# Kernel optimization log

Measured on AMD Instinct MI355X. Metric: run time of the kernel, lower is better.

## Reference

```python
import jax, jax.numpy as jnp
import numpy as np

NUM_HEADS = 8
NUM_GROUPS = 32
EPS = 1e-5


def setup_inputs() -> dict:
    key = jax.random.key(0)
    ks = jax.random.split(key, 7)
    B, C, H, W = 8, 512, 32, 32
    x = jax.random.normal(ks[0], (B, C, H, W), dtype=jnp.float32)
    # GroupNorm affine params
    gn_w = jnp.ones((C,), dtype=jnp.float32)
    gn_b = jnp.zeros((C,), dtype=jnp.float32)
    # 1x1 conv == linear over channel dim; store squeezed weights (out, in)
    qkv_w = jax.random.normal(ks[1], (3 * C, C), dtype=jnp.float32) * (1.0 / np.sqrt(C))
    qkv_b = jnp.zeros((3 * C,), dtype=jnp.float32)
    proj_w = jax.random.normal(ks[2], (C, C), dtype=jnp.float32) * (1.0 / np.sqrt(C))
    proj_b = jnp.zeros((C,), dtype=jnp.float32)
    return {"x": x, "gn_w": gn_w, "gn_b": gn_b, "qkv_w": qkv_w,
            "qkv_b": qkv_b, "proj_w": proj_w, "proj_b": proj_b}


def reference(x, gn_w, gn_b, qkv_w, qkv_b, proj_w, proj_b):
    B, C, H, W = x.shape
    G = NUM_GROUPS
    hd = C // NUM_HEADS
    scale = hd ** -0.5
    # GroupNorm: normalize over (C//G, H, W) per group
    xg = x.reshape(B, G, C // G, H, W)
    mean = xg.mean(axis=(2, 3, 4), keepdims=True)
    var = xg.var(axis=(2, 3, 4), keepdims=True)
    xn = ((xg - mean) * jax.lax.rsqrt(var + EPS)).reshape(B, C, H, W)
    xn = xn * gn_w[None, :, None, None] + gn_b[None, :, None, None]
    # QKV 1x1 conv
    qkv = jnp.einsum('bchw,oc->bohw', xn, qkv_w) + qkv_b[None, :, None, None]
    # (B, 3, heads, head_dim, HW) -> (3, B, heads, HW, head_dim)
    qkv = qkv.reshape(B, 3, NUM_HEADS, hd, H * W).transpose(1, 0, 2, 4, 3)
    q, k, v = qkv[0], qkv[1], qkv[2]
    attn = jax.nn.softmax(jnp.einsum('bhqd,bhkd->bhqk', q, k) * scale, axis=-1)
    out = jnp.einsum('bhqk,bhkd->bhqd', attn, v)  # (B, heads, HW, hd)
    out = out.transpose(0, 1, 3, 2).reshape(B, C, H, W)
    out = jnp.einsum('bchw,oc->bohw', out, proj_w) + proj_b[None, :, None, None]
    return out + x
```

## Files before the change

kernel.cpp:

```cpp
#include <hip/hip_runtime.h>
#include <hip/hip_bf16.h>
#include <math.h>

typedef __bf16 bf16_t;
typedef __bf16 bf16x8 __attribute__((ext_vector_type(8)));
typedef __bf16 bf16x4 __attribute__((ext_vector_type(4)));
typedef float  f32x4  __attribute__((ext_vector_type(4)));
typedef short  short4v __attribute__((ext_vector_type(4)));

#define NB    8
#define NC    512
#define NHW   1024
#define NHEAD 8
#define NHD   64
#define NG    32
#define NCG   16
#define NO3   1536

__device__ __forceinline__ void lds_load16(bf16_t* lds, const bf16_t* g) {
  __builtin_amdgcn_global_load_lds(
      (__attribute__((address_space(1))) unsigned int*)(g),
      (__attribute__((address_space(3))) unsigned int*)(void*)(lds),
      16, 0, 0);
}

__device__ __forceinline__ f32x4 mfma16(bf16x4 a, bf16x4 b, f32x4 c) {
#if __has_builtin(__builtin_amdgcn_mfma_f32_16x16x16bf16_1k)
  return __builtin_amdgcn_mfma_f32_16x16x16bf16_1k(
      __builtin_bit_cast(short4v, a), __builtin_bit_cast(short4v, b), c, 0, 0, 0);
#else
  f32x4 d;
  asm("v_mfma_f32_16x16x16_bf16 %0, %1, %2, %3"
      : "=v"(d) : "v"(a), "v"(b), "v"(c));
  return d;
#endif
}

__global__ __launch_bounds__(256)
void gn_kernel(const float* __restrict__ x, const float* __restrict__ gw,
               const float* __restrict__ gb, bf16_t* __restrict__ xn)
{
  const int bg = blockIdx.x;
  const int b = bg >> 5, g = bg & 31;
  const float* xp = x + ((size_t)b * NC + g * NCG) * NHW;
  const int tid = threadIdx.x;
  const int wave = tid >> 6, lane = tid & 63;

  float s1 = 0.f, s2 = 0.f;
  const float4* xp4 = (const float4*)xp;
  for (int i = tid; i < 4096; i += 256) {
    float4 v = xp4[i];
    s1 += v.x + v.y + v.z + v.w;
    s2 += v.x * v.x + v.y * v.y + v.z * v.z + v.w * v.w;
  }
  for (int off = 32; off > 0; off >>= 1) {
    s1 += __shfl_down(s1, off);
    s2 += __shfl_down(s2, off);
  }
  __shared__ float red[16];
  if (lane == 0) { red[wave] = s1; red[8 + wave] = s2; }
  __syncthreads();
  float tot1 = red[0] + red[1] + red[2] + red[3];
  float tot2 = red[8] + red[9] + red[10] + red[11];
  const float mean = tot1 * (1.0f / 16384.0f);
  const float var  = tot2 * (1.0f / 16384.0f) - mean * mean;
  const float rstd = rsqrtf(var + 1e-5f);

  float gam[NCG], bet[NCG];
  #pragma unroll
  for (int c = 0; c < NCG; ++c) {
    gam[c] = gw[g * NCG + c] * rstd;
    bet[c] = gb[g * NCG + c] - mean * gam[c];
  }
  bf16_t* op = xn + (size_t)b * NHW * NC + g * NCG;
  for (int s = tid; s < NHW; s += 256) {
    __align__(16) bf16_t vals[NCG];
    #pragma unroll
    for (int c = 0; c < NCG; ++c)
      vals[c] = (bf16_t)(xp[c * NHW + s] * gam[c] + bet[c]);
    *(bf16x8*)(op + (size_t)s * NC)     = *(const bf16x8*)&vals[0];
    *(bf16x8*)(op + (size_t)s * NC + 8) = *(const bf16x8*)&vals[8];
  }
}

__global__ __launch_bounds__(256)
void wconv_kernel(const float* __restrict__ qw, const float* __restrict__ pw,
                  bf16_t* __restrict__ qwb, bf16_t* __restrict__ pwb)
{
  const int gid = blockIdx.x * 256 + threadIdx.x;
  const int n1 = NO3 * NC / 4;
  float4 v; bf16x4 o;
  if (gid < n1) {
    v = ((const float4*)qw)[gid];
    o[0] = (bf16_t)v.x; o[1] = (bf16_t)v.y; o[2] = (bf16_t)v.z; o[3] = (bf16_t)v.w;
    ((bf16x4*)qwb)[gid] = o;
  } else {
    int g2 = gid - n1;
    v = ((const float4*)pw)[g2];
    o[0] = (bf16_t)v.x; o[1] = (bf16_t)v.y; o[2] = (bf16_t)v.z; o[3] = (bf16_t)v.w;
    ((bf16x4*)pwb)[g2] = o;
  }
}

__device__ __forceinline__ void gemm_mainloop(const bf16_t* Ap, const bf16_t* Bp,
                                              bf16_t* sA, bf16_t* sB, f32x4 (&acc)[4][4])
{
  const int tid = threadIdx.x;
  const int wave = tid >> 6, lane = tid & 63;
  const int quad = lane >> 4, l16 = lane & 15;
  const int wm = wave >> 1, wn = wave & 1;
  for (int k0 = 0; k0 < 512; k0 += 32) {
    #pragma unroll
    for (int j = 0; j < 2; ++j) {
      int c = wave * 64 + j * 256 + lane;
      int row = c >> 2, ko = (c & 3) * 8;
      lds_load16(sA + (size_t)(wave * 64 + j * 256) * 8, Ap + (size_t)row * 512 + k0 + ko);
      lds_load16(sB + (size_t)(wave * 64 + j * 256) * 8, Bp + (size_t)row * 512 + k0 + ko);
    }
    __syncthreads();
    bf16x8 af[4], bfr[4];
    #pragma unroll
    for (int mi = 0; mi < 4; ++mi)
      af[mi] = *(const bf16x8*)(sA + (wm * 64 + mi * 16 + l16) * 32 + quad * 8);
    #pragma unroll
    for (int ni = 0; ni < 4; ++ni)
      bfr[ni] = *(const bf16x8*)(sB + (wn * 64 + ni * 16 + l16) * 32 + quad * 8);
    #pragma unroll
    for (int mi = 0; mi < 4; ++mi)
      #pragma unroll
      for (int ni = 0; ni < 4; ++ni)
        acc[mi][ni] = __builtin_amdgcn_mfma_f32_16x16x32_bf16(af[mi], bfr[ni], acc[mi][ni], 0, 0, 0);
    __syncthreads();
  }
}

__global__ __launch_bounds__(256, 2)
void qkv_gemm(const bf16_t* __restrict__ xn, const bf16_t* __restrict__ w,
              const float* __restrict__ bias,
              bf16_t* __restrict__ qbuf, bf16_t* __restrict__ kbuf, bf16_t* __restrict__ vbuf)
{
  __shared__ __align__(16) bf16_t smem[128 * 136];
  bf16_t* sA = smem;
  bf16_t* sB = smem + 4096;
  const int tid = threadIdx.x;
  const int wave = tid >> 6, lane = tid & 63;
  const int quad = lane >> 4, l16 = lane & 15;
  const int wm = wave >> 1, wn = wave & 1;
  const int bx = blockIdx.x, by = blockIdx.y, b = blockIdx.z;

  const bf16_t* Ap = xn + ((size_t)b * NHW + by * 128) * NC;
  const bf16_t* Bp = w + (size_t)bx * 128 * NC;
  f32x4 acc[4][4] = {};
  gemm_mainloop(Ap, Bp, sA, sB, acc);

  const int obase = bx * 128 + wn * 64;
  const int sbase = by * 128 + wm * 64;
  float bv[4];
  #pragma unroll
  for (int ni = 0; ni < 4; ++ni) bv[ni] = bias[obase + ni * 16 + l16];

  if (bx < 8) {
    const bool isq = (bx < 4);
    bf16_t* basep = isq ? qbuf : kbuf;
    const float scale = isq ? 0.18033688f : 1.0f;
    #pragma unroll
    for (int ni = 0; ni < 4; ++ni) {
      int o = obase + ni * 16 + l16;
      int hh = (o >> 6) & 7, dd = o & 63;
      bf16_t* dst = basep + ((size_t)(b * NHEAD + hh) * NHW) * NHD + dd;
      #pragma unroll
      for (int mi = 0; mi < 4; ++mi)
        #pragma unroll
        for (int r = 0; r < 4; ++r) {
          int s = sbase + mi * 16 + quad * 4 + r;
          dst[(size_t)s * NHD] = (bf16_t)((acc[mi][ni][r] + bv[ni]) * scale);
        }
    }
  } else {
    bf16_t* sC = smem;
    __syncthreads();
    #pragma unroll
    for (int ni = 0; ni < 4; ++ni)
      #pragma unroll
      for (int mi = 0; mi < 4; ++mi)
        #pragma unroll
        for (int r = 0; r < 4; ++r)
          sC[(wn * 64 + ni * 16 + l16) * 136 + wm * 64 + mi * 16 + quad * 4 + r] =
              (bf16_t)(acc[mi][ni][r] + bv[ni]);
    __syncthreads();
    int o_local = tid >> 1, shalf = (tid & 1) << 6;
    int ov = (bx - 8) * 128 + o_local;
    int hh = ov >> 6, dd = ov & 63;
    bf16_t* dst = vbuf + ((size_t)(b * NHEAD + hh) * NHD + dd) * NHW + by * 128 + shalf;
    #pragma unroll
    for (int jj = 0; jj < 8; ++jj)
      *(bf16x8*)(dst + jj * 8) = *(const bf16x8*)&sC[o_local * 136 + shalf + jj * 8];
  }
}

__global__ __launch_bounds__(256, 2)
void attn_kernel(const bf16_t* __restrict__ qbuf, const bf16_t* __restrict__ kbuf,
                 const bf16_t* __restrict__ vbuf, bf16_t* __restrict__ obuf)
{
  __shared__ __align__(16) char smem_raw[36864];
  bf16_t* Ks = (bf16_t*)smem_raw;
  bf16_t* Vs = (bf16_t*)(smem_raw + 18432);
  f32x4*  mO = (f32x4*)smem_raw;
  float*  mM = (float*)(smem_raw + 32768);
  float*  mL = mM + 256;

  const int tid = threadIdx.x;
  const int wave = tid >> 6, lane = tid & 63;
  const int quad = lane >> 4, l16 = lane & 15;
  const int wl = wave & 1;
  const int wg = wave >> 1;
  const int mtb = wg * 4;
  const int idx = blockIdx.x;
  const int qt = idx >> 6, h = (idx >> 3) & 7, b = idx & 7;
  const size_t bh = (size_t)b * NHEAD + h;
  const bf16_t* qp = qbuf + (bh * NHW + qt * 64 + wl * 32) * NHD;
  const bf16_t* kp = kbuf + bh * NHW * NHD;
  const bf16_t* vp = vbuf + bh * NHD * NHW;

  bf16x8 qf[2][2];
  #pragma unroll
  for (int stile = 0; stile < 2; ++stile)
    #pragma unroll
    for (int kc = 0; kc < 2; ++kc)
      qf[stile][kc] = *(const bf16x8*)(qp + (size_t)(stile * 16 + l16) * NHD + kc * 32 + quad * 8);

  float m_i[2] = {-1e30f, -1e30f}, l_i[2] = {0.f, 0.f};
  f32x4 oacc[4][2] = {};

  bf16x8 kreg[4], vreg[4];
  {
    const bf16_t* ksrc = kp;
    const bf16_t* vsrc = vp;
    #pragma unroll
    for (int j = 0; j < 4; ++j) {
      int c = tid + j * 256;
      kreg[j] = *(const bf16x8*)(ksrc + (size_t)(c >> 3) * NHD + (c & 7) * 8);
      vreg[j] = *(const bf16x8*)(vsrc + (size_t)(c >> 4) * NHW + (c & 15) * 8);
    }
  }

  for (int kt = 0; kt < 8; ++kt) {
    __syncthreads();
    #pragma unroll
    for (int j = 0; j < 4; ++j) {
      int c = tid + j * 256;
      *(bf16x8*)&Ks[(c >> 3) * 72 + (c & 7) * 8]  = kreg[j];
      *(bf16x8*)&Vs[(c >> 4) * 136 + (c & 15) * 8] = vreg[j];
    }
    __syncthreads();
    if (kt < 7) {
      const bf16_t* ksrc = kp + (size_t)(kt + 1) * 128 * NHD;
      const bf16_t* vsrc = vp + (kt + 1) * 128;
      #pragma unroll
      for (int j = 0; j < 4; ++j) {
        int c = tid + j * 256;
        kreg[j] = *(const bf16x8*)(ksrc + (size_t)(c >> 3) * NHD + (c & 7) * 8);
        vreg[j] = *(const bf16x8*)(vsrc + (size_t)(c >> 4) * NHW + (c & 15) * 8);
      }
    }

    f32x4 st[2][4];
    #pragma unroll
    for (int mt = 0; mt < 4; ++mt) {
      int mtg = mtb + mt;
      bf16x8 ka0 = *(const bf16x8*)&Ks[(mtg * 16 + l16) * 72 + quad * 8];
      bf16x8 ka1 = *(const bf16x8*)&Ks[(mtg * 16 + l16) * 72 + 32 + quad * 8];
      #pragma unroll
      for (int stile = 0; stile < 2; ++stile) {
        f32x4 z = {};
        z = __builtin_amdgcn_mfma_f32_16x16x32_bf16(ka0, qf[stile][0], z, 0, 0, 0);
        z = __builtin_amdgcn_mfma_f32_16x16x32_bf16(ka1, qf[stile][1], z, 0, 0, 0);
        st[stile][mt] = z;
      }
    }

    #pragma unroll
    for (int stile = 0; stile < 2; ++stile) {
      float mx = -1e30f;
      #pragma unroll
      for (int mt = 0; mt < 4; ++mt)
        #pragma unroll
        for (int r = 0; r < 4; ++r) mx = fmaxf(mx, st[stile][mt][r]);
      mx = fmaxf(mx, __shfl_xor(mx, 16));
      mx = fmaxf(mx, __shfl_xor(mx, 32));
      float mnew = fmaxf(m_i[stile], mx);
      float alpha = exp2f(m_i[stile] - mnew);
      m_i[stile] = mnew;
      float rs = 0.f;
      #pragma unroll
      for (int mt = 0; mt < 4; ++mt)
        #pragma unroll
        for (int r = 0; r < 4; ++r) {
          float p = exp2f(st[stile][mt][r] - mnew);
          rs += p;
          st[stile][mt][r] = p;
        }
      rs += __shfl_xor(rs, 16);
      rs += __shfl_xor(rs, 32);
      l_i[stile] = l_i[stile] * alpha + rs;
      #pragma unroll
      for (int mi = 0; mi < 4; ++mi)
        #pragma unroll
        for (int r = 0; r < 4; ++r)
          oacc[mi][stile][r] *= alpha;
    }

    #pragma unroll
    for (int mt = 0; mt < 4; ++mt) {
      int mtg = mtb + mt;
      bf16x4 pb[2];
      #pragma unroll
      for (int stile = 0; stile < 2; ++stile) {
        pb[stile][0] = (bf16_t)st[stile][mt][0];
        pb[stile][1] = (bf16_t)st[stile][mt][1];
        pb[stile][2] = (bf16_t)st[stile][mt][2];
        pb[stile][3] = (bf16_t)st[stile][mt][3];
      }
      #pragma unroll
      for (int mi = 0; mi < 4; ++mi) {
        bf16x4 va = *(const bf16x4*)&Vs[(mi * 16 + l16) * 136 + mtg * 16 + quad * 4];
        oacc[mi][0] = mfma16(va, pb[0], oacc[mi][0]);
        oacc[mi][1] = mfma16(va, pb[1], oacc[mi][1]);
      }
    }
  }

  __syncthreads();
  if (wg == 1) {
    #pragma unroll
    for (int stile = 0; stile < 2; ++stile) {
      mM[(wl * 2 + stile) * 64 + lane] = m_i[stile];
      mL[(wl * 2 + stile) * 64 + lane] = l_i[stile];
      #pragma unroll
      for (int mi = 0; mi < 4; ++mi)
        mO[((wl * 2 + stile) * 4 + mi) * 64 + lane] = oacc[mi][stile];
    }
  }
  __syncthreads();
  if (wg == 0) {
    #pragma unroll
    for (int stile = 0; stile < 2; ++stile) {
      float mB = mM[(wl * 2 + stile) * 64 + lane];
      float lB = mL[(wl * 2 + stile) * 64 + lane];
      float mS = fmaxf(m_i[stile], mB);
      float aA = exp2f(m_i[stile] - mS);
      float aB = exp2f(mB - mS);
      float inv = 1.0f / (l_i[stile] * aA + lB * aB);
      int s = qt * 64 + wl * 32 + stile * 16 + l16;
      bf16_t* orow = obuf + ((size_t)b * NHW + s) * NC + h * NHD;
      #pragma unroll
      for (int mi = 0; mi < 4; ++mi) {
        f32x4 oB = mO[((wl * 2 + stile) * 4 + mi) * 64 + lane];
        __align__(8) bf16_t o4[4];
        #pragma unroll
        for (int r = 0; r < 4; ++r)
          o4[r] = (bf16_t)((oacc[mi][stile][r] * aA + oB[r] * aB) * inv);
        *(bf16x4*)(orow + mi * 16 + quad * 4) = *(const bf16x4*)o4;
      }
    }
  }
}

__global__ __launch_bounds__(256, 2)
void proj_gemm(const bf16_t* __restrict__ ob, const bf16_t* __restrict__ w,
               const float* __restrict__ bias, const float* __restrict__ x,
               float* __restrict__ out)
{
  __shared__ __align__(16) bf16_t smem[8192];
  bf16_t* sA = smem;
  bf16_t* sB = smem + 4096;
  const int tid = threadIdx.x;
  const int wave = tid >> 6, lane = tid & 63;
  const int quad = lane >> 4, l16 = lane & 15;
  const int wm = wave >> 1, wn = wave & 1;
  const int bx = blockIdx.x, by = blockIdx.y, b = blockIdx.z;

  const bf16_t* Ap = w + (size_t)by * 128 * NC;
  const bf16_t* Bp = ob + ((size_t)b * NHW + bx * 128) * NC;
  f32x4 acc[4][4] = {};
  gemm_mainloop(Ap, Bp, sA, sB, acc);

  const int cobase = by * 128 + wm * 64;
  const int sbase  = bx * 128 + wn * 64;
  #pragma unroll
  for (int mi = 0; mi < 4; ++mi)
    #pragma unroll
    for (int r = 0; r < 4; ++r) {
      int co = cobase + mi * 16 + quad * 4 + r;
      float pb = bias[co];
      const float* xrow = x + ((size_t)b * NC + co) * NHW;
      float* orow = out + ((size_t)b * NC + co) * NHW;
      #pragma unroll
      for (int ni = 0; ni < 4; ++ni) {
        int s = sbase + ni * 16 + l16;
        orow[s] = acc[mi][ni][r] + pb + xrow[s];
      }
    }
}

extern "C" void kernel_launch(void* const* d_in, const int* in_sizes, int n_in,
                              void* d_out, int out_size, void* d_ws, size_t ws_size,
                              hipStream_t stream)
{
  const float* x      = (const float*)d_in[0];
  const float* gn_w   = (const float*)d_in[1];
  const float* gn_b   = (const float*)d_in[2];
  const float* qkv_w  = (const float*)d_in[3];
  const float* qkv_b  = (const float*)d_in[4];
  const float* proj_w = (const float*)d_in[5];
  const float* proj_b = (const float*)d_in[6];
  float* out = (float*)d_out;

  char* ws = (char*)d_ws;
  bf16_t* xn   = (bf16_t*)(ws);
  bf16_t* qwb  = (bf16_t*)(ws + 8388608);
  bf16_t* pwb  = (bf16_t*)(ws + 9961472);
  bf16_t* qbuf = (bf16_t*)(ws + 10485760);
  bf16_t* kbuf = (bf16_t*)(ws + 18874368);
  bf16_t* vbuf = (bf16_t*)(ws + 27262976);
  bf16_t* obuf = xn;

  gn_kernel<<<dim3(NB * NG), dim3(256), 0, stream>>>(x, gn_w, gn_b, xn);
  wconv_kernel<<<dim3(1024), dim3(256), 0, stream>>>(qkv_w, proj_w, qwb, pwb);
  qkv_gemm<<<dim3(12, 8, NB), dim3(256), 0, stream>>>(xn, qwb, qkv_b, qbuf, kbuf, vbuf);
  attn_kernel<<<dim3(1024), dim3(256), 0, stream>>>(qbuf, kbuf, vbuf, obuf);
  proj_gemm<<<dim3(8, 4, NB), dim3(256), 0, stream>>>(obuf, pwb, proj_b, x, out);
}
```

Baseline: 170.2 us.

## Double-buffer K/V via direct global-to-LDS loads with swizzle and lazy rescale

The attention loop now uses a 64-key tile, double-buffered in LDS and filled with global_load_lds direct copies. This replaces the register staging with two barriers per iteration. LDS layout uses an XOR swizzle instead of padding to avoid bank conflicts. Online-softmax rescaling is skipped when no lane's max increases, and the row-sum reduction across lanes is deferred to the end. MFMA sections get raised wave priority. Together these cut synchronisation and shuffle overhead but double the number of iterations.

```diff
diff --git a/kernel.cpp b/kernel.cpp
--- a/kernel.cpp
+++ b/kernel.cpp
@@ -16,6 +16,8 @@
 #define NG    32
 #define NCG   16
 #define NO3   1536
+#define KVB   64
+#define NKT   16
 
 __device__ __forceinline__ void lds_load16(bf16_t* lds, const bf16_t* g) {
   __builtin_amdgcn_global_load_lds(
@@ -202,25 +204,25 @@
 void attn_kernel(const bf16_t* __restrict__ qbuf, const bf16_t* __restrict__ kbuf,
                  const bf16_t* __restrict__ vbuf, bf16_t* __restrict__ obuf)
 {
-  __shared__ __align__(16) char smem_raw[36864];
-  bf16_t* Ks = (bf16_t*)smem_raw;
-  bf16_t* Vs = (bf16_t*)(smem_raw + 18432);
-  f32x4*  mO = (f32x4*)smem_raw;
-  float*  mM = (float*)(smem_raw + 32768);
-  float*  mL = mM + 256;
+  __shared__ __align__(16) char smem[32768];
+  f32x4* mO = (f32x4*)smem;
+  float* mM = (float*)(smem + 16384);
+  float* mL = (float*)(smem + 17408);
 
   const int tid = threadIdx.x;
   const int wave = tid >> 6, lane = tid & 63;
   const int quad = lane >> 4, l16 = lane & 15;
   const int wl = wave & 1;
   const int wg = wave >> 1;
-  const int mtb = wg * 4;
   const int idx = blockIdx.x;
   const int qt = idx >> 6, h = (idx >> 3) & 7, b = idx & 7;
   const size_t bh = (size_t)b * NHEAD + h;
   const bf16_t* qp = qbuf + (bh * NHW + qt * 64 + wl * 32) * NHD;
-  const bf16_t* kp = kbuf + bh * NHW * NHD;
-  const bf16_t* vp = vbuf + bh * NHD * NHW;
+  const char* kp = (const char*)(kbuf + bh * NHW * NHD);
+  const char* vp = (const char*)(vbuf + bh * NHD * NHW);
+
+  const int r8 = lane >> 3;
+  const int swc = (((lane & 7) << 4)) ^ (r8 << 4);
 
   bf16x8 qf[2][2];
   #pragma unroll
@@ -229,47 +231,46 @@
     for (int kc = 0; kc < 2; ++kc)
       qf[stile][kc] = *(const bf16x8*)(qp + (size_t)(stile * 16 + l16) * NHD + kc * 32 + quad * 8);
 
-  float m_i[2] = {-1e30f, -1e30f}, l_i[2] = {0.f, 0.f};
+  float m_i[2] = {-1e30f, -1e30f};
+  float ll[2] = {0.f, 0.f};
   f32x4 oacc[4][2] = {};
 
-  bf16x8 kreg[4], vreg[4];
-  {
-    const bf16_t* ksrc = kp;
-    const bf16_t* vsrc = vp;
-    #pragma unroll
-    for (int j = 0; j < 4; ++j) {
-      int c = tid + j * 256;
-      kreg[j] = *(const bf16x8*)(ksrc + (size_t)(c >> 3) * NHD + (c & 7) * 8);
-      vreg[j] = *(const bf16x8*)(vsrc + (size_t)(c >> 4) * NHW + (c & 15) * 8);
-    }
-  }
-
-  for (int kt = 0; kt < 8; ++kt) {
-    __syncthreads();
-    #pragma unroll
-    for (int j = 0; j < 4; ++j) {
-      int c = tid + j * 256;
-      *(bf16x8*)&Ks[(c >> 3) * 72 + (c & 7) * 8]  = kreg[j];
-      *(bf16x8*)&Vs[(c >> 4) * 136 + (c & 15) * 8] = vreg[j];
-    }
-    __syncthreads();
-    if (kt < 7) {
-      const bf16_t* ksrc = kp + (size_t)(kt + 1) * 128 * NHD;
-      const bf16_t* vsrc = vp + (kt + 1) * 128;
-      #pragma unroll
-      for (int j = 0; j < 4; ++j) {
-        int c = tid + j * 256;
-        kreg[j] = *(const bf16x8*)(ksrc + (size_t)(c >> 3) * NHD + (c & 7) * 8);
-        vreg[j] = *(const bf16x8*)(vsrc + (size_t)(c >> 4) * NHW + (c & 15) * 8);
-      }
-    }
-
-    f32x4 st[2][4];
-    #pragma unroll
-    for (int mt = 0; mt < 4; ++mt) {
-      int mtg = mtb + mt;
-      bf16x8 ka0 = *(const bf16x8*)&Ks[(mtg * 16 + l16) * 72 + quad * 8];
-      bf16x8 ka1 = *(const bf16x8*)&Ks[(mtg * 16 + l16) * 72 + 32 + quad * 8];
+  #pragma unroll
+  for (int j = 0; j < 2; ++j) {
+    int i = wave * 2 + j;
+    const char* kg = kp + ((size_t)(i * 8 + r8) * NHD) * 2 + swc;
+    lds_load16((bf16_t*)(smem + i * 1024), (const bf16_t*)kg);
+    const char* vg = vp + ((size_t)(i * 8 + r8) * NHW) * 2 + swc;
+    lds_load16((bf16_t*)(smem + 8192 + i * 1024), (const bf16_t*)vg);
+  }
+  __syncthreads();
+
+  const int swr = (l16 & 7) << 4;
+
+  for (int kt = 0; kt < NKT; ++kt) {
+    const int cur = kt & 1;
+    const char* Kb = smem + cur * 16384;
+    const char* Vb = Kb + 8192;
+    if (kt < NKT - 1) {
+      char* Kn = smem + (cur ^ 1) * 16384;
+      #pragma unroll
+      for (int j = 0; j < 2; ++j) {
+        int i = wave * 2 + j;
+        const char* kg = kp + ((size_t)((kt + 1) * KVB + i * 8 + r8) * NHD) * 2 + swc;
+        lds_load16((bf16_t*)(Kn + i * 1024), (const bf16_t*)kg);
+        const char* vg = vp + ((size_t)(i * 8 + r8) * NHW + (kt + 1) * KVB) * 2 + swc;
+        lds_load16((bf16_t*)(Kn + 8192 + i * 1024), (const bf16_t*)vg);
+      }
+    }
+
+    f32x4 st[2][2];
+    __builtin_amdgcn_s_setprio(1);
+    #pragma unroll
+    for (int mt = 0; mt < 2; ++mt) {
+      const int mtg = wg * 2 + mt;
+      const char* krow = Kb + (mtg * 16 + l16) * 128;
+      bf16x8 ka0 = *(const bf16x8*)(krow + ((quad * 16) ^ swr));
+      bf16x8 ka1 = *(const bf16x8*)(krow + ((64 + quad * 16) ^ swr));
       #pragma unroll
       for (int stile = 0; stile < 2; ++stile) {
         f32x4 z = {};
@@ -278,41 +279,43 @@
         st[stile][mt] = z;
       }
     }
+    __builtin_amdgcn_s_setprio(0);
 
     #pragma unroll
     for (int stile = 0; stile < 2; ++stile) {
-      float mx = -1e30f;
-      #pragma unroll
-      for (int mt = 0; mt < 4; ++mt)
+      float mx = st[stile][0][0];
+      #pragma unroll
+      for (int mt = 0; mt < 2; ++mt)
         #pragma unroll
         for (int r = 0; r < 4; ++r) mx = fmaxf(mx, st[stile][mt][r]);
-      mx = fmaxf(mx, __shfl_xor(mx, 16));
-      mx = fmaxf(mx, __shfl_xor(mx, 32));
-      float mnew = fmaxf(m_i[stile], mx);
-      float alpha = exp2f(m_i[stile] - mnew);
-      m_i[stile] = mnew;
+      if (!__all(mx <= m_i[stile])) {
+        mx = fmaxf(mx, __shfl_xor(mx, 16));
+        mx = fmaxf(mx, __shfl_xor(mx, 32));
+        float mnew = fmaxf(m_i[stile], mx);
+        float alpha = exp2f(m_i[stile] - mnew);
+        m_i[stile] = mnew;
+        ll[stile] *= alpha;
+        #pragma unroll
+        for (int mi = 0; mi < 4; ++mi)
+          #pragma unroll
+          for (int r = 0; r < 4; ++r) oacc[mi][stile][r] *= alpha;
+      }
       float rs = 0.f;
       #pragma unroll
-      for (int mt = 0; mt < 4; ++mt)
+      for (int mt = 0; mt < 2; ++mt)
         #pragma unroll
         for (int r = 0; r < 4; ++r) {
-          float p = exp2f(st[stile][mt][r] - mnew);
+          float p = exp2f(st[stile][mt][r] - m_i[stile]);
           rs += p;
           st[stile][mt][r] = p;
         }
-      rs += __shfl_xor(rs, 16);
-      rs += __shfl_xor(rs, 32);
-      l_i[stile] = l_i[stile] * alpha + rs;
-      #pragma unroll
-      for (int mi = 0; mi < 4; ++mi)
-        #pragma unroll
-        for (int r = 0; r < 4; ++r)
-          oacc[mi][stile][r] *= alpha;
-    }
-
-    #pragma unroll
-    for (int mt = 0; mt < 4; ++mt) {
-      int mtg = mtb + mt;
+      ll[stile] += rs;
+    }
+
+    __builtin_amdgcn_s_setprio(1);
+    #pragma unroll
+    for (int mt = 0; mt < 2; ++mt) {
+      const int mtg = wg * 2 + mt;
       bf16x4 pb[2];
       #pragma unroll
       for (int stile = 0; stile < 2; ++stile) {
@@ -323,14 +326,25 @@
       }
       #pragma unroll
       for (int mi = 0; mi < 4; ++mi) {
-        bf16x4 va = *(const bf16x4*)&Vs[(mi * 16 + l16) * 136 + mtg * 16 + quad * 4];
+        const char* vrow = Vb + (mi * 16 + l16) * 128;
+        bf16x4 va = *(const bf16x4*)(vrow + ((mtg * 32 + quad * 8) ^ swr));
         oacc[mi][0] = mfma16(va, pb[0], oacc[mi][0]);
         oacc[mi][1] = mfma16(va, pb[1], oacc[mi][1]);
       }
     }
-  }
-
-  __syncthreads();
+    __builtin_amdgcn_s_setprio(0);
+    __syncthreads();
+  }
+
+  float l_i[2];
+  #pragma unroll
+  for (int stile = 0; stile < 2; ++stile) {
+    float rs = ll[stile];
+    rs += __shfl_xor(rs, 16);
+    rs += __shfl_xor(rs, 32);
+    l_i[stile] = rs;
+  }
+
   if (wg == 1) {
     #pragma unroll
     for (int stile = 0; stile < 2; ++stile) {
```

New measurement: 173.2 us. About the same (+1.8%).
